# Kernel tuning notes

Hardware: AMD Instinct MI355X
Metric: run time of the kernel (lower is better)

The kernel has to match this reference:

```python
import jax, jax.numpy as jnp
import numpy as np

NUM_HEADS = 16
LN_EPS = 1e-5


def _transpose_qkv(X, num_heads):
    # Faithful to the repo's (buggy) transpose_qkv:
    # (B,S,D) -> (B,S,H,D/H) -> permute (B,H,S,D/H) -> reshape (B,S,D)
    B, S, D = X.shape
    X = X.reshape(B, S, num_heads, D // num_heads)
    X = jnp.transpose(X, (0, 2, 1, 3))
    return X.reshape(B, S, D)


def _layer_norm(x, w, b):
    mu = jnp.mean(x, axis=-1, keepdims=True)
    var = jnp.var(x, axis=-1, keepdims=True)
    return (x - mu) * jax.lax.rsqrt(var + LN_EPS) * w + b


def setup_inputs() -> dict:
    key = jax.random.key(0)
    ks = jax.random.split(key, 4)
    B, S, D = 4, 2048, 1024
    scale = 1.0 / np.sqrt(D)
    return {
        "src": jax.random.normal(ks[0], (B, S, D), dtype=jnp.float32),
        "W_q": jax.random.normal(ks[1], (D, D), dtype=jnp.float32) * scale,
        "W_k": jax.random.normal(ks[2], (D, D), dtype=jnp.float32) * scale,
        "W_v": jax.random.normal(ks[3], (D, D), dtype=jnp.float32) * scale,
        "ln1_w": jnp.ones((D,), dtype=jnp.float32),
        "ln1_b": jnp.zeros((D,), dtype=jnp.float32),
        "ln2_w": jnp.ones((D,), dtype=jnp.float32),
        "ln2_b": jnp.zeros((D,), dtype=jnp.float32),
    }


def reference(src, W_q, W_k, W_v, ln1_w, ln1_b, ln2_w, ln2_b):
    # W_* stored as (in, out): y = x @ W  (equivalent to torch Linear, bias=False)
    q = _transpose_qkv(src @ W_q, NUM_HEADS)  # (B,S,D)
    k = _transpose_qkv(src @ W_k, NUM_HEADS)
    v = _transpose_qkv(src @ W_v, NUM_HEADS)
    d = q.shape[-1]  # note: full hidden dim, per the buggy transpose_qkv
    scores = jnp.einsum("bqd,bkd->bqk", q, k) / jnp.sqrt(jnp.float32(d))
    a = jax.nn.softmax(scores, axis=-1)          # (B,S,S) attention weights
    att = jnp.einsum("bqk,bkd->bqd", a, v)       # (B,S,D)
    src2 = _layer_norm(att, ln1_w, ln1_b)        # norm1
    X = _layer_norm(src + src2, ln2_w, ln2_b)    # AddNorm (dropout=0 in eval)
    return (X, a)
```

## Files before the change

### kernel.cpp

```cpp
#include <hip/hip_runtime.h>

typedef _Float16 f16;
typedef __attribute__((ext_vector_type(2))) _Float16 f16x2;
typedef __attribute__((ext_vector_type(4))) _Float16 f16x4;
typedef __attribute__((ext_vector_type(8))) _Float16 f16x8;
typedef __attribute__((ext_vector_type(4))) float f32x4;

#define D_MODEL 1024
#define SEQ 2048
#define NBATCH 4
#define NROWS (NBATCH * SEQ)

__device__ __forceinline__ void gload16(const void* g, void* l) {
  __builtin_amdgcn_global_load_lds(
      (__attribute__((address_space(1))) void*)(void*)g,
      (__attribute__((address_space(3))) void*)l, 16, 0, 0);
}

#define BARF                                   \
  do {                                         \
    asm volatile("" ::: "memory");             \
    __builtin_amdgcn_s_barrier();              \
    asm volatile("" ::: "memory");             \
  } while (0)
#define PRIO1 __builtin_amdgcn_s_setprio(1)
#define PRIO0 __builtin_amdgcn_s_setprio(0)

template <int BN>
__device__ __forceinline__ void gemm8_core(
    const f16* aP0, const f16* aP1, const f16* aP2, const f16* aP3,
    const f16* bP0, const f16* bP1, const f16* bP2, const f16* bP3,
    int stepA, int stepB, int NT, f16* lds, f32x4* acc)
{
  constexpr int NJ = BN / 128;
  constexpr int NACC = 2 * NJ;
  constexpr int SLOT = 16384 + BN * 64;
  const int t = threadIdx.x, l = t & 63;
  const int w = t >> 6, wm = w >> 2, wn = w & 3;
  const int fr = l & 15, g0 = l >> 4;

  int aof[2][4][2], bof[2][NJ][2];
#pragma unroll
  for (int mh = 0; mh < 2; ++mh)
#pragma unroll
    for (int mi = 0; mi < 4; ++mi)
#pragma unroll
      for (int kh = 0; kh < 2; ++kh) {
        const int ra = wm * 128 + mh * 64 + mi * 16 + fr;
        aof[mh][mi][kh] = ra * 64 + (((g0 + kh * 4) ^ (ra & 7)) << 3);
      }
#pragma unroll
  for (int nh = 0; nh < 2; ++nh)
#pragma unroll
    for (int j = 0; j < NJ; ++j)
#pragma unroll
      for (int kh = 0; kh < 2; ++kh) {
        const int rb = (BN == 256) ? (wn * 64 + fr * 4 + nh * 2 + j)
                                   : (wn * 32 + fr * 2 + nh);
        bof[nh][j][kh] = rb * 64 + (((g0 + kh * 4) ^ ((rb >> 2) & 7)) << 3);
      }
#pragma unroll
  for (int i = 0; i < 8 * NACC; ++i) acc[i] = f32x4{0.f, 0.f, 0.f, 0.f};

  f16x8 fa[4][2];
  f16x8 fb[2][NJ][2];

#define STAGE_A(SL)                                  \
  {                                                  \
    f16* d = lds + (SL) * SLOT + t * 8;              \
    gload16(aP0, d);                                 \
    gload16(aP1, d + 4096);                          \
    gload16(aP2, d + 8192);                          \
    gload16(aP3, d + 12288);                         \
  }
#define STAGE_B(SL)                                  \
  {                                                  \
    f16* d = lds + (SL) * SLOT + 16384 + t * 8;      \
    gload16(bP0, d);                                 \
    gload16(bP1, d + 4096);                          \
    if constexpr (BN == 256) {                       \
      gload16(bP2, d + 8192);                        \
      gload16(bP3, d + 12288);                       \
    }                                                \
  }
#define ADVA { aP0 += stepA; aP1 += stepA; aP2 += stepA; aP3 += stepA; }
#define ADVB                                         \
  {                                                  \
    bP0 += stepB; bP1 += stepB;                      \
    if constexpr (BN == 256) { bP2 += stepB; bP3 += stepB; } \
  }
#define VMC                                                        \
  if constexpr (BN == 256) {                                       \
    asm volatile("s_waitcnt vmcnt(4)" ::: "memory");               \
  } else {                                                         \
    asm volatile("s_waitcnt vmcnt(2)" ::: "memory");               \
  }
#define LOAD_A(MH)                                   \
  _Pragma("unroll") for (int mi = 0; mi < 4; ++mi)   \
  _Pragma("unroll") for (int kh = 0; kh < 2; ++kh)   \
      fa[mi][kh] = *(const f16x8*)(LA + aof[MH][mi][kh]);
#define LOAD_B(NH)                                   \
  _Pragma("unroll") for (int j = 0; j < NJ; ++j)     \
  _Pragma("unroll") for (int kh = 0; kh < 2; ++kh)   \
      fb[NH][j][kh] = *(const f16x8*)(LBp + bof[NH][j][kh]);
#define MFMA_BLK(MH, NH)                                                    \
  _Pragma("unroll") for (int mi = 0; mi < 4; ++mi)                          \
  _Pragma("unroll") for (int j = 0; j < NJ; ++j)                            \
  _Pragma("unroll") for (int kh = 0; kh < 2; ++kh)                          \
      acc[((MH)*4 + mi) * NACC + (NH)*NJ + j] =                             \
          __builtin_amdgcn_mfma_f32_16x16x32_f16(                           \
              fa[mi][kh], fb[NH][j][kh],                                    \
              acc[((MH)*4 + mi) * NACC + (NH)*NJ + j], 0, 0, 0);

  (void)bP2; (void)bP3;
  STAGE_A(0); ADVA;
  STAGE_B(0); ADVB;
  STAGE_B(1); ADVB;
  VMC;
  BARF;

  for (int kt = 0; kt < NT; ++kt) {
    const int sl = kt & 1;
    const f16* LA = lds + sl * SLOT;
    const f16* LBp = LA + 16384;
    STAGE_A(sl ^ 1);
    if (kt + 2 < NT) ADVA;
    LOAD_A(0); LOAD_B(0); LOAD_B(1);
    PRIO1; MFMA_BLK(0, 0); MFMA_BLK(0, 1); PRIO0;
    BARF;
    LOAD_A(1);
    STAGE_B(sl);
    if (kt + 3 < NT) ADVB;
    VMC;
    PRIO1; MFMA_BLK(1, 0); MFMA_BLK(1, 1); PRIO0;
    BARF;
  }
#undef STAGE_A
#undef STAGE_B
#undef ADVA
#undef ADVB
#undef VMC
#undef LOAD_A
#undef LOAD_B
#undef MFMA_BLK
}

__global__ __launch_bounds__(512, 2) void k_qkv3(
    const f16* __restrict__ srch, const f16* __restrict__ wt,
    f16* __restrict__ qp, f16* __restrict__ kp, f16* __restrict__ vp)
{
  __shared__ f16 lds[2 * (16384 + 128 * 64)];
  const int t = threadIdx.x, l = t & 63;
  const int w = t >> 6, wm = w >> 2, wn = w & 3;
  const int fr = l & 15, g0 = l >> 4, c = t & 7;
  const int z = blockIdx.y >> 3, cb = blockIdx.y & 7;
  const f16 *aP[4], *bP[2];
#pragma unroll
  for (int i = 0; i < 4; ++i) {
    const int rl = i * 64 + (t >> 3);
    aP[i] = srch + (size_t)(blockIdx.x * 256 + rl) * 1024 + ((c ^ (rl & 7)) << 3);
  }
#pragma unroll
  for (int i = 0; i < 2; ++i) {
    const int rl = i * 64 + (t >> 3);
    bP[i] = wt + ((size_t)z << 20) + (size_t)(cb * 128 + rl) * 1024 +
            ((c ^ ((rl >> 2) & 7)) << 3);
  }
  f32x4 acc[16];
  gemm8_core<128>(aP[0], aP[1], aP[2], aP[3], bP[0], bP[1], bP[0], bP[0],
                  64, 64, 16, lds, acc);
  f16* dst = (z == 0) ? qp : (z == 1 ? kp : vp);
  const int col = cb * 128 + wn * 32 + fr * 2;
#pragma unroll
  for (int mi = 0; mi < 8; ++mi)
#pragma unroll
    for (int q = 0; q < 4; ++q) {
      const int row = blockIdx.x * 256 + wm * 128 + mi * 16 + g0 * 4 + q;
      f16x2 o = {(f16)acc[mi * 2 + 0][q], (f16)acc[mi * 2 + 1][q]};
      *(f16x2*)(dst + (size_t)row * 1024 + col) = o;
    }
}

__global__ __launch_bounds__(512, 2) void k_scores(
    const f16* __restrict__ qp, const f16* __restrict__ kp,
    f16* __restrict__ abf)
{
  __shared__ f16 lds[2 * (16384 + 256 * 64)];
  const int t = threadIdx.x, l = t & 63;
  const int w = t >> 6, wm = w >> 2, wn = w & 3;
  const int fr = l & 15, g0 = l >> 4, c = t & 7;
  const int b = blockIdx.z;
  const f16* qb = qp + ((size_t)b << 21);
  const f16* kb = kp + ((size_t)b << 21);
  const f16 *aP[4], *bP[4];
#pragma unroll
  for (int i = 0; i < 4; ++i) {
    const int rl = i * 64 + (t >> 3);
    const int spA = blockIdx.x * 256 + rl;
    aP[i] = qb + (size_t)((spA & 127) << 4) * 1024 + ((spA >> 7) << 6) +
            ((c ^ (rl & 7)) << 3);
    const int spB = blockIdx.y * 256 + rl;
    bP[i] = kb + (size_t)((spB & 127) << 4) * 1024 + ((spB >> 7) << 6) +
            ((c ^ ((rl >> 2) & 7)) << 3);
  }
  f32x4 acc[32];
  gemm8_core<256>(aP[0], aP[1], aP[2], aP[3], bP[0], bP[1], bP[2], bP[3],
                  1024, 1024, 16, lds, acc);
  f16* Cb = abf + ((size_t)b << 22);
  const int col = blockIdx.y * 256 + wn * 64 + fr * 4;
#pragma unroll
  for (int mi = 0; mi < 8; ++mi)
#pragma unroll
    for (int q = 0; q < 4; ++q) {
      const int row = blockIdx.x * 256 + wm * 128 + mi * 16 + g0 * 4 + q;
      f16x4 o = {(f16)(acc[mi * 4 + 0][q] * 0.03125f),
                 (f16)(acc[mi * 4 + 1][q] * 0.03125f),
                 (f16)(acc[mi * 4 + 2][q] * 0.03125f),
                 (f16)(acc[mi * 4 + 3][q] * 0.03125f)};
      *(f16x4*)(Cb + (size_t)row * 2048 + col) = o;
    }
}

__global__ __launch_bounds__(512, 2) void k_att(
    const f16* __restrict__ abf, const f16* __restrict__ vtT,
    f16* __restrict__ attb)
{
  __shared__ f16 lds[2 * (16384 + 128 * 64)];
  const int t = threadIdx.x, l = t & 63;
  const int w = t >> 6, wm = w >> 2, wn = w & 3;
  const int fr = l & 15, g0 = l >> 4, c = t & 7;
  const int b = blockIdx.z;
  const f16* ab = abf + ((size_t)b << 22);
  const f16* vb = vtT + ((size_t)b << 21);
  const f16 *aP[4], *bP[2];
#pragma unroll
  for (int i = 0; i < 4; ++i) {
    const int rl = i * 64 + (t >> 3);
    aP[i] = ab + (size_t)(blockIdx.x * 256 + rl) * 2048 + ((c ^ (rl & 7)) << 3);
  }
#pragma unroll
  for (int i = 0; i < 2; ++i) {
    const int rl = i * 64 + (t >> 3);
    bP[i] = vb + (size_t)(blockIdx.y * 128 + rl) * 2048 +
            ((c ^ ((rl >> 2) & 7)) << 3);
  }
  f32x4 acc[16];
  gemm8_core<128>(aP[0], aP[1], aP[2], aP[3], bP[0], bP[1], bP[0], bP[0],
                  64, 64, 32, lds, acc);
  f16* Cb = attb + ((size_t)b << 21);
  const int col = blockIdx.y * 128 + wn * 32 + fr * 2;
#pragma unroll
  for (int mi = 0; mi < 8; ++mi)
#pragma unroll
    for (int q = 0; q < 4; ++q) {
      const int row = blockIdx.x * 256 + wm * 128 + mi * 16 + g0 * 4 + q;
      f16x2 o = {(f16)acc[mi * 2 + 0][q], (f16)acc[mi * 2 + 1][q]};
      *(f16x2*)(Cb + (size_t)row * 1024 + col) = o;
    }
}

__global__ __launch_bounds__(256) void k_scrT(const f16* __restrict__ vp,
                                              f16* __restrict__ vtT)
{
  __shared__ f16 tile[64][68];
  const int t = threadIdx.x;
  const int sp0 = blockIdx.x * 64, dp0 = blockIdx.y * 64;
  const int d6 = dp0 >> 6;
  const int jb = (sp0 >> 7) << 6;
  const int sbase = sp0 & 127;
  const f16* src = vp + ((size_t)blockIdx.z << 21);
  f16* dst = vtT + ((size_t)blockIdx.z << 21);
#pragma unroll
  for (int p = 0; p < 2; ++p) {
    const int u = p * 32 + (t >> 3);
    const int s = ((sbase + u) << 4) | d6;
    const int c = (t & 7) << 3;
    f16x8 v = *(const f16x8*)(src + (size_t)s * 1024 + jb + c);
    *(f16x4*)&tile[u][c]     = f16x4{v[0], v[1], v[2], v[3]};
    *(f16x4*)&tile[u][c + 4] = f16x4{v[4], v[5], v[6], v[7]};
  }
  __syncthreads();
#pragma unroll
  for (int p = 0; p < 2; ++p) {
    const int cc = p * 32 + (t >> 3);
    const int v0 = (t & 7) << 3;
    f16x8 o;
#pragma unroll
    for (int j = 0; j < 8; ++j) o[j] = tile[v0 + j][cc];
    *(f16x8*)(dst + (size_t)(dp0 + cc) * 2048 + sp0 + v0) = o;
  }
}

__global__ __launch_bounds__(256) void k_cast_f16(const float* __restrict__ in,
                                                  f16* __restrict__ out)
{
  const size_t i = (size_t)blockIdx.x * 256 + threadIdx.x;
  const float4* p = (const float4*)in;
  float4 v0 = p[2 * i], v1 = p[2 * i + 1];
  f16x8 o;
  o[0] = (f16)v0.x; o[1] = (f16)v0.y; o[2] = (f16)v0.z; o[3] = (f16)v0.w;
  o[4] = (f16)v1.x; o[5] = (f16)v1.y; o[6] = (f16)v1.z; o[7] = (f16)v1.w;
  *(f16x8*)(out + 8 * i) = o;
}

__global__ __launch_bounds__(256) void k_castT(
    const float* __restrict__ w0, const float* __restrict__ w1,
    const float* __restrict__ w2, f16* __restrict__ out)
{
  const float* in = (blockIdx.z == 0) ? w0 : (blockIdx.z == 1 ? w1 : w2);
  f16* o = out + ((size_t)blockIdx.z << 20);
  __shared__ f16 tile[64][65];
  const int t = threadIdx.x;
  const int rr = t >> 4, c4 = (t & 15) * 4;
  const int r0 = blockIdx.x * 64, c0 = blockIdx.y * 64;
#pragma unroll
  for (int i = 0; i < 4; ++i) {
    float4 f = *(const float4*)(in + (size_t)(r0 + rr + 16 * i) * 1024 + c0 + c4);
    tile[rr + 16 * i][c4 + 0] = (f16)f.x;
    tile[rr + 16 * i][c4 + 1] = (f16)f.y;
    tile[rr + 16 * i][c4 + 2] = (f16)f.z;
    tile[rr + 16 * i][c4 + 3] = (f16)f.w;
  }
  __syncthreads();
#pragma unroll
  for (int i = 0; i < 4; ++i) {
    const int n = c0 + rr + 16 * i;
    f16* dst = o + (size_t)n * 1024 + r0 + c4;
    dst[0] = tile[c4 + 0][rr + 16 * i];
    dst[1] = tile[c4 + 1][rr + 16 * i];
    dst[2] = tile[c4 + 2][rr + 16 * i];
    dst[3] = tile[c4 + 3][rr + 16 * i];
  }
}

__global__ __launch_bounds__(256) void k_softmax(float* __restrict__ out,
                                                 f16* __restrict__ abf)
{
  const size_t base = (size_t)blockIdx.x * 2048;
  const int t = threadIdx.x, lane = t & 63, w = t >> 6;
  f16x8 v = *(const f16x8*)(abf + base + (size_t)t * 8);
  float x[8];
#pragma unroll
  for (int j = 0; j < 8; ++j) x[j] = (float)v[j];
  float m = fmaxf(fmaxf(fmaxf(x[0], x[1]), fmaxf(x[2], x[3])),
                  fmaxf(fmaxf(x[4], x[5]), fmaxf(x[6], x[7])));
#pragma unroll
  for (int off = 1; off < 64; off <<= 1) m = fmaxf(m, __shfl_xor(m, off));
  __shared__ float red[8];
  if (lane == 0) red[w] = m;
  __syncthreads();
  m = fmaxf(fmaxf(red[0], red[1]), fmaxf(red[2], red[3]));
  float s = 0.f;
#pragma unroll
  for (int j = 0; j < 8; ++j) { x[j] = __expf(x[j] - m); s += x[j]; }
#pragma unroll
  for (int off = 1; off < 64; off <<= 1) s += __shfl_xor(s, off);
  if (lane == 0) red[4 + w] = s;
  __syncthreads();
  s = red[4] + red[5] + red[6] + red[7];
  const float inv = 1.0f / s;
#pragma unroll
  for (int j = 0; j < 8; ++j) x[j] *= inv;
  float4 o0 = {x[0], x[1], x[2], x[3]}, o1 = {x[4], x[5], x[6], x[7]};
  ((float4*)(out + base))[2 * t] = o0;
  ((float4*)(out + base))[2 * t + 1] = o1;
  f16x8 ov;
#pragma unroll
  for (int j = 0; j < 8; ++j) ov[j] = (f16)x[j];
  *(f16x8*)(abf + base + (size_t)t * 8) = ov;
}

__global__ __launch_bounds__(256) void k_ln(
    const f16* __restrict__ attb, const float* __restrict__ src,
    const float* __restrict__ w1, const float* __restrict__ b1,
    const float* __restrict__ w2, const float* __restrict__ b2,
    float* __restrict__ out)
{
  const size_t base = (size_t)blockIdx.x * 1024;
  const int t = threadIdx.x, lane = t & 63, w = t >> 6;
  f16x4 a4 = ((const f16x4*)(attb + base))[t];
  float ax = (float)a4[0], ay = (float)a4[1], az = (float)a4[2], aw = (float)a4[3];
  float s = ax + ay + az + aw;
  float s2 = ax * ax + ay * ay + az * az + aw * aw;
#pragma unroll
  for (int off = 1; off < 64; off <<= 1) {
    s += __shfl_xor(s, off);
    s2 += __shfl_xor(s2, off);
  }
  __shared__ float red[16];
  if (lane == 0) { red[w] = s; red[4 + w] = s2; }
  __syncthreads();
  s = red[0] + red[1] + red[2] + red[3];
  s2 = red[4] + red[5] + red[6] + red[7];
  float mu = s * (1.0f / 1024.0f);
  float var = s2 * (1.0f / 1024.0f) - mu * mu;
  float rs = rsqrtf(var + 1e-5f);
  float4 W1 = ((const float4*)w1)[t], B1 = ((const float4*)b1)[t];
  float4 sv = ((const float4*)(src + base))[t];
  float y0 = sv.x + (ax - mu) * rs * W1.x + B1.x;
  float y1 = sv.y + (ay - mu) * rs * W1.y + B1.y;
  float y2 = sv.z + (az - mu) * rs * W1.z + B1.z;
  float y3 = sv.w + (aw - mu) * rs * W1.w + B1.w;
  s = y0 + y1 + y2 + y3;
  s2 = y0 * y0 + y1 * y1 + y2 * y2 + y3 * y3;
#pragma unroll
  for (int off = 1; off < 64; off <<= 1) {
    s += __shfl_xor(s, off);
    s2 += __shfl_xor(s2, off);
  }
  if (lane == 0) { red[8 + w] = s; red[12 + w] = s2; }
  __syncthreads();
  s = red[8] + red[9] + red[10] + red[11];
  s2 = red[12] + red[13] + red[14] + red[15];
  mu = s * (1.0f / 1024.0f);
  var = s2 * (1.0f / 1024.0f) - mu * mu;
  rs = rsqrtf(var + 1e-5f);
  float4 W2 = ((const float4*)w2)[t], B2 = ((const float4*)b2)[t];
  float4 o;
  o.x = (y0 - mu) * rs * W2.x + B2.x;
  o.y = (y1 - mu) * rs * W2.y + B2.y;
  o.z = (y2 - mu) * rs * W2.z + B2.z;
  o.w = (y3 - mu) * rs * W2.w + B2.w;
  ((float4*)(out + base))[t] = o;
}

extern "C" void kernel_launch(void* const* d_in, const int* in_sizes, int n_in,
                              void* d_out, int out_size, void* d_ws, size_t ws_size,
                              hipStream_t stream) {
  const float* src = (const float*)d_in[0];
  const float* Wq  = (const float*)d_in[1];
  const float* Wk  = (const float*)d_in[2];
  const float* Wv  = (const float*)d_in[3];
  const float* l1w = (const float*)d_in[4];
  const float* l1b = (const float*)d_in[5];
  const float* l2w = (const float*)d_in[6];
  const float* l2b = (const float*)d_in[7];
  float* Xout = (float*)d_out;
  float* Aout = Xout + (size_t)NROWS * D_MODEL;

  char* ws = (char*)d_ws;
  f16* srch = (f16*)ws;
  f16* wt   = (f16*)(ws + (16u << 20));
  f16* qp   = (f16*)(ws + (22u << 20));
  f16* kp   = (f16*)(ws + (38u << 20));
  f16* vp   = (f16*)(ws + (54u << 20));
  f16* vtT  = (f16*)(ws + (70u << 20));
  f16* abf  = (f16*)(ws + (86u << 20));
  f16* attb = (f16*)(ws + (118u << 20));

  k_cast_f16<<<4096, 256, 0, stream>>>(src, srch);
  k_castT<<<dim3(16, 16, 3), 256, 0, stream>>>(Wq, Wk, Wv, wt);
  k_qkv3<<<dim3(32, 24), 512, 0, stream>>>(srch, wt, qp, kp, vp);
  k_scrT<<<dim3(32, 16, 4), 256, 0, stream>>>(vp, vtT);
  k_scores<<<dim3(8, 8, 4), 512, 0, stream>>>(qp, kp, abf);
  k_softmax<<<NROWS, 256, 0, stream>>>(Aout, abf);
  k_att<<<dim3(8, 8, 4), 512, 0, stream>>>(abf, vtT, attb);
  k_ln<<<NROWS, 256, 0, stream>>>(attb, src, l1w, l1b, l2w, l2b, Xout);
}
```

Before: 201.4 us.

## Restructure GEMM core into 8-phase half-tile ping-pong pipeline

Replaces the two-phase double-buffered GEMM mainloop with an eight-phase schedule. LDS is split into half-tiles per operand and buffer, global-to-LDS staging is interleaved with LDS fragment reads and MFMA quadrants, and explicit lgkmcnt waits plus barriers sit between phases. The aim is finer overlap of global loads, LDS reads and matrix math across the waves. In exchange it adds many more barriers per k-step and a new buffer-indexing scheme. The LDS sizes are unchanged.

```diff
diff --git a/kernel.cpp b/kernel.cpp
--- a/kernel.cpp
+++ b/kernel.cpp
@@ -23,133 +23,160 @@
     __builtin_amdgcn_s_barrier();              \
     asm volatile("" ::: "memory");             \
   } while (0)
+#define LGK asm volatile("s_waitcnt lgkmcnt(0)" ::: "memory")
 #define PRIO1 __builtin_amdgcn_s_setprio(1)
 #define PRIO0 __builtin_amdgcn_s_setprio(0)
 
+
+#define STAGE_A(D, H)                                        \
+  {                                                          \
+    f16* d_ = lds + ((D) * 2 + (H)) * 8192 + t * 8;          \
+    gload16((H) ? aP2 : aP0, d_);                            \
+    gload16((H) ? aP3 : aP1, d_ + 4096);                     \
+  }
+#define STAGE_B(D, H)                                        \
+  {                                                          \
+    if constexpr (BN == 256) {                               \
+      f16* d_ = lds + 32768 + ((D) * 2 + (H)) * 8192 + t * 8;\
+      gload16((H) ? bP2 : bP0, d_);                          \
+      gload16((H) ? bP3 : bP1, d_ + 4096);                   \
+    } else {                                                 \
+      f16* d_ = lds + 32768 + (D) * 8192 + t * 8;            \
+      gload16(bP0, d_);                                      \
+      gload16(bP1, d_ + 4096);                               \
+    }                                                        \
+  }
+#define ADVA                                                 \
+  {                                                          \
+    if (ka < NT - 1) {                                       \
+      ka++;                                                  \
+      aP0 += stepA; aP1 += stepA; aP2 += stepA; aP3 += stepA;\
+    }                                                        \
+  }
+#define ADVB                                                 \
+  {                                                          \
+    if (kb < NT - 1) {                                       \
+      kb++;                                                  \
+      bP0 += stepB; bP1 += stepB;                            \
+      if constexpr (BN == 256) { bP2 += stepB; bP3 += stepB; } \
+    }                                                        \
+  }
+#define VMC_STEADY                                           \
+  {                                                          \
+    if constexpr (BN == 256) {                               \
+      asm volatile("s_waitcnt vmcnt(4)" ::: "memory");       \
+    } else {                                                 \
+      asm volatile("s_waitcnt vmcnt(2)" ::: "memory");       \
+    }                                                        \
+  }
+#define RD_A(D, MH)                                          \
+  _Pragma("unroll") for (int mi = 0; mi < 4; ++mi)           \
+  _Pragma("unroll") for (int kh = 0; kh < 2; ++kh) {         \
+    const int rr = (MH) * 64 + mi * 16 + fr;                 \
+    fa[mi][kh] = *(const f16x8*)(lds + ((D) * 2 + wm) * 8192 \
+        + rr * 64 + (((g0 + kh * 4) ^ (rr & 7)) << 3));      \
+  }
+#define RD_B(D, NH)                                          \
+  _Pragma("unroll") for (int j = 0; j < NJ; ++j)             \
+  _Pragma("unroll") for (int kh = 0; kh < 2; ++kh) {         \
+    int rbr, base;                                           \
+    if constexpr (BN == 256) {                               \
+      rbr = (wn & 1) * 64 + fr * 4 + (NH) * 2 + j;           \
+      base = 32768 + ((D) * 2 + (wn >> 1)) * 8192;           \
+    } else {                                                 \
+      rbr = wn * 32 + fr * 2 + (NH);                         \
+      base = 32768 + (D) * 8192;                             \
+    }                                                        \
+    fb[NH][j][kh] = *(const f16x8*)(lds + base + rbr * 64 +  \
+        (((g0 + kh * 4) ^ ((rbr >> 2) & 7)) << 3));          \
+  }
+#define MFMA_Q(MH, NH)                                       \
+  _Pragma("unroll") for (int mi = 0; mi < 4; ++mi)           \
+  _Pragma("unroll") for (int j = 0; j < NJ; ++j)             \
+  _Pragma("unroll") for (int kh = 0; kh < 2; ++kh)           \
+    acc[((MH) * 4 + mi) * 2 * NJ + (NH) * NJ + j] =          \
+        __builtin_amdgcn_mfma_f32_16x16x32_f16(              \
+            fa[mi][kh], fb[NH][j][kh],                       \
+            acc[((MH) * 4 + mi) * 2 * NJ + (NH) * NJ + j], 0, 0, 0);
+
 template <int BN>
-__device__ __forceinline__ void gemm8_core(
+__device__ __forceinline__ void gemm8p(
     const f16* aP0, const f16* aP1, const f16* aP2, const f16* aP3,
     const f16* bP0, const f16* bP1, const f16* bP2, const f16* bP3,
     int stepA, int stepB, int NT, f16* lds, f32x4* acc)
 {
   constexpr int NJ = BN / 128;
-  constexpr int NACC = 2 * NJ;
-  constexpr int SLOT = 16384 + BN * 64;
   const int t = threadIdx.x, l = t & 63;
   const int w = t >> 6, wm = w >> 2, wn = w & 3;
   const int fr = l & 15, g0 = l >> 4;
-
-  int aof[2][4][2], bof[2][NJ][2];
-#pragma unroll
-  for (int mh = 0; mh < 2; ++mh)
-#pragma unroll
-    for (int mi = 0; mi < 4; ++mi)
-#pragma unroll
-      for (int kh = 0; kh < 2; ++kh) {
-        const int ra = wm * 128 + mh * 64 + mi * 16 + fr;
-        aof[mh][mi][kh] = ra * 64 + (((g0 + kh * 4) ^ (ra & 7)) << 3);
-      }
-#pragma unroll
-  for (int nh = 0; nh < 2; ++nh)
-#pragma unroll
-    for (int j = 0; j < NJ; ++j)
-#pragma unroll
-      for (int kh = 0; kh < 2; ++kh) {
-        const int rb = (BN == 256) ? (wn * 64 + fr * 4 + nh * 2 + j)
-                                   : (wn * 32 + fr * 2 + nh);
-        bof[nh][j][kh] = rb * 64 + (((g0 + kh * 4) ^ ((rb >> 2) & 7)) << 3);
-      }
-#pragma unroll
-  for (int i = 0; i < 8 * NACC; ++i) acc[i] = f32x4{0.f, 0.f, 0.f, 0.f};
-
-  f16x8 fa[4][2];
-  f16x8 fb[2][NJ][2];
-
-#define STAGE_A(SL)                                  \
-  {                                                  \
-    f16* d = lds + (SL) * SLOT + t * 8;              \
-    gload16(aP0, d);                                 \
-    gload16(aP1, d + 4096);                          \
-    gload16(aP2, d + 8192);                          \
-    gload16(aP3, d + 12288);                         \
-  }
-#define STAGE_B(SL)                                  \
-  {                                                  \
-    f16* d = lds + (SL) * SLOT + 16384 + t * 8;      \
-    gload16(bP0, d);                                 \
-    gload16(bP1, d + 4096);                          \
-    if constexpr (BN == 256) {                       \
-      gload16(bP2, d + 8192);                        \
-      gload16(bP3, d + 12288);                       \
-    }                                                \
-  }
-#define ADVA { aP0 += stepA; aP1 += stepA; aP2 += stepA; aP3 += stepA; }
-#define ADVB                                         \
-  {                                                  \
-    bP0 += stepB; bP1 += stepB;                      \
-    if constexpr (BN == 256) { bP2 += stepB; bP3 += stepB; } \
-  }
-#define VMC                                                        \
-  if constexpr (BN == 256) {                                       \
-    asm volatile("s_waitcnt vmcnt(4)" ::: "memory");               \
-  } else {                                                         \
-    asm volatile("s_waitcnt vmcnt(2)" ::: "memory");               \
-  }
-#define LOAD_A(MH)                                   \
-  _Pragma("unroll") for (int mi = 0; mi < 4; ++mi)   \
-  _Pragma("unroll") for (int kh = 0; kh < 2; ++kh)   \
-      fa[mi][kh] = *(const f16x8*)(LA + aof[MH][mi][kh]);
-#define LOAD_B(NH)                                   \
-  _Pragma("unroll") for (int j = 0; j < NJ; ++j)     \
-  _Pragma("unroll") for (int kh = 0; kh < 2; ++kh)   \
-      fb[NH][j][kh] = *(const f16x8*)(LBp + bof[NH][j][kh]);
-#define MFMA_BLK(MH, NH)                                                    \
-  _Pragma("unroll") for (int mi = 0; mi < 4; ++mi)                          \
-  _Pragma("unroll") for (int j = 0; j < NJ; ++j)                            \
-  _Pragma("unroll") for (int kh = 0; kh < 2; ++kh)                          \
-      acc[((MH)*4 + mi) * NACC + (NH)*NJ + j] =                             \
-          __builtin_amdgcn_mfma_f32_16x16x32_f16(                           \
-              fa[mi][kh], fb[NH][j][kh],                                    \
-              acc[((MH)*4 + mi) * NACC + (NH)*NJ + j], 0, 0, 0);
-
+  f16x8 fa[4][2], fb[2][NJ][2];
+#pragma unroll
+  for (int i = 0; i < 8 * 2 * NJ; ++i) acc[i] = f32x4{0.f, 0.f, 0.f, 0.f};
+  int ka = 0, kb = 0;
   (void)bP2; (void)bP3;
-  STAGE_A(0); ADVA;
-  STAGE_B(0); ADVB;
-  STAGE_B(1); ADVB;
-  VMC;
+
+  STAGE_A(0, 0); STAGE_A(0, 1); ADVA;
+  if constexpr (BN == 256) { STAGE_B(0, 0); STAGE_B(0, 1); }
+  else { STAGE_B(0, 0); }
+  ADVB;
+  if constexpr (BN == 256) { STAGE_B(1, 0); STAGE_B(1, 1); }
+  else { STAGE_B(1, 0); }
+  ADVB;
+  VMC_STEADY;
   BARF;
 
-  for (int kt = 0; kt < NT; ++kt) {
-    const int sl = kt & 1;
-    const f16* LA = lds + sl * SLOT;
-    const f16* LBp = LA + 16384;
-    STAGE_A(sl ^ 1);
-    if (kt + 2 < NT) ADVA;
-    LOAD_A(0); LOAD_B(0); LOAD_B(1);
-    PRIO1; MFMA_BLK(0, 0); MFMA_BLK(0, 1); PRIO0;
-    BARF;
-    LOAD_A(1);
-    STAGE_B(sl);
-    if (kt + 3 < NT) ADVB;
-    VMC;
-    PRIO1; MFMA_BLK(1, 0); MFMA_BLK(1, 1); PRIO0;
-    BARF;
-  }
-#undef STAGE_A
-#undef STAGE_B
-#undef ADVA
-#undef ADVB
-#undef VMC
-#undef LOAD_A
-#undef LOAD_B
-#undef MFMA_BLK
+#pragma unroll 1
+  for (int it = 0; it < NT / 2; ++it) {
+    RD_A(0, 0); RD_B(0, 0);
+    STAGE_A(1, 0);
+    BARF; LGK;
+    PRIO1; MFMA_Q(0, 0); PRIO0;
+    BARF;
+    RD_B(0, 1);
+    STAGE_A(1, 1); ADVA;
+    BARF; LGK;
+    PRIO1; MFMA_Q(0, 1); PRIO0;
+    BARF;
+    RD_A(0, 1);
+    STAGE_B(0, 0);
+    if constexpr (BN == 128) ADVB;
+    BARF; LGK;
+    PRIO1; MFMA_Q(1, 0); PRIO0;
+    BARF;
+    if constexpr (BN == 256) { STAGE_B(0, 1); ADVB; }
+    VMC_STEADY;
+    BARF;
+    PRIO1; MFMA_Q(1, 1); PRIO0;
+    BARF;
+    RD_A(1, 0); RD_B(1, 0);
+    STAGE_A(0, 0);
+    BARF; LGK;
+    PRIO1; MFMA_Q(0, 0); PRIO0;
+    BARF;
+    RD_B(1, 1);
+    STAGE_A(0, 1); ADVA;
+    BARF; LGK;
+    PRIO1; MFMA_Q(0, 1); PRIO0;
+    BARF;
+    RD_A(1, 1);
+    STAGE_B(1, 0);
+    if constexpr (BN == 128) ADVB;
+    BARF; LGK;
+    PRIO1; MFMA_Q(1, 0); PRIO0;
+    BARF;
+    if constexpr (BN == 256) { STAGE_B(1, 1); ADVB; }
+    VMC_STEADY;
+    BARF;
+    PRIO1; MFMA_Q(1, 1); PRIO0;
+    BARF;
+  }
 }
 
 __global__ __launch_bounds__(512, 2) void k_qkv3(
     const f16* __restrict__ srch, const f16* __restrict__ wt,
     f16* __restrict__ qp, f16* __restrict__ kp, f16* __restrict__ vp)
 {
-  __shared__ f16 lds[2 * (16384 + 128 * 64)];
+  __shared__ f16 lds[49152];
   const int t = threadIdx.x, l = t & 63;
   const int w = t >> 6, wm = w >> 2, wn = w & 3;
   const int fr = l & 15, g0 = l >> 4, c = t & 7;
@@ -167,8 +194,8 @@
             ((c ^ ((rl >> 2) & 7)) << 3);
   }
   f32x4 acc[16];
-  gemm8_core<128>(aP[0], aP[1], aP[2], aP[3], bP[0], bP[1], bP[0], bP[0],
-                  64, 64, 16, lds, acc);
+  gemm8p<128>(aP[0], aP[1], aP[2], aP[3], bP[0], bP[1], bP[0], bP[0],
+              64, 64, 16, lds, acc);
   f16* dst = (z == 0) ? qp : (z == 1 ? kp : vp);
   const int col = cb * 128 + wn * 32 + fr * 2;
 #pragma unroll
@@ -185,7 +212,7 @@
     const f16* __restrict__ qp, const f16* __restrict__ kp,
     f16* __restrict__ abf)
 {
-  __shared__ f16 lds[2 * (16384 + 256 * 64)];
+  __shared__ f16 lds[65536];
   const int t = threadIdx.x, l = t & 63;
   const int w = t >> 6, wm = w >> 2, wn = w & 3;
   const int fr = l & 15, g0 = l >> 4, c = t & 7;
@@ -204,8 +231,8 @@
             ((c ^ ((rl >> 2) & 7)) << 3);
   }
   f32x4 acc[32];
-  gemm8_core<256>(aP[0], aP[1], aP[2], aP[3], bP[0], bP[1], bP[2], bP[3],
-                  1024, 1024, 16, lds, acc);
+  gemm8p<256>(aP[0], aP[1], aP[2], aP[3], bP[0], bP[1], bP[2], bP[3],
+              1024, 1024, 16, lds, acc);
   f16* Cb = abf + ((size_t)b << 22);
   const int col = blockIdx.y * 256 + wn * 64 + fr * 4;
 #pragma unroll
@@ -225,7 +252,7 @@
     const f16* __restrict__ abf, const f16* __restrict__ vtT,
     f16* __restrict__ attb)
 {
-  __shared__ f16 lds[2 * (16384 + 128 * 64)];
+  __shared__ f16 lds[49152];
   const int t = threadIdx.x, l = t & 63;
   const int w = t >> 6, wm = w >> 2, wn = w & 3;
   const int fr = l & 15, g0 = l >> 4, c = t & 7;
@@ -245,8 +272,8 @@
             ((c ^ ((rl >> 2) & 7)) << 3);
   }
   f32x4 acc[16];
-  gemm8_core<128>(aP[0], aP[1], aP[2], aP[3], bP[0], bP[1], bP[0], bP[0],
-                  64, 64, 32, lds, acc);
+  gemm8p<128>(aP[0], aP[1], aP[2], aP[3], bP[0], bP[1], bP[0], bP[0],
+              64, 64, 32, lds, acc);
   f16* Cb = attb + ((size_t)b << 21);
   const int col = blockIdx.y * 128 + wn * 32 + fr * 2;
 #pragma unroll
```

After: 199.8 us. About the same (-0.8%).
